# Kernel optimization log

Hardware: AMD Instinct MI355X
Metric: run time of the kernel (lower is better)

The kernel has to match this reference:

```python
import jax, jax.numpy as jnp
import numpy as np

B, L, D, H, N, F_, DM = 16, 2048, 128, 4, 4, 129, 16
DK = D // H
DFF = 2 * D
INT = int(np.sqrt(D))  # 11
V = F_ + 1


def _uinit(key, shape, fan):
    s = float(np.sqrt(6.0 / fan))
    return jax.random.uniform(key, shape, jnp.float32, -s, s)


def setup_inputs() -> dict:
    key = jax.random.key(0)
    ks = jax.random.split(key, 24)
    return {
        "values": jax.random.normal(ks[0], (B, L), jnp.float32),
        "times": jax.random.uniform(ks[1], (B, L), jnp.float32),
        "variables": jax.random.randint(ks[2], (B, L), 0, F_),
        "input_mask": jax.random.randint(ks[3], (B, L), 0, 2).astype(bool),
        "demographics": jax.random.normal(ks[4], (B, DM), jnp.float32),
        # CVE time
        "W1t": _uinit(ks[5], (1, INT), 1 + INT), "b1t": jnp.zeros((INT,), jnp.float32),
        "W2t": _uinit(ks[6], (INT, D), INT + D),
        # CVE value
        "W1v": _uinit(ks[7], (1, INT), 1 + INT), "b1v": jnp.zeros((INT,), jnp.float32),
        "W2v": _uinit(ks[8], (INT, D), INT + D),
        # variable embedding table
        "var_table": jax.random.normal(ks[9], (V, D), jnp.float32),
        # transformer stacks (init_proj: uniform(-s, s), s = sqrt(6/(fan_in+fan_out)) of last two dims)
        "Wq": _uinit(ks[10], (N, H, D, DK), D + DK),
        "Wk": _uinit(ks[11], (N, H, D, DK), D + DK),
        "Wv": _uinit(ks[12], (N, H, D, DK), D + DK),
        "Wo": _uinit(ks[13], (N, D, D), 2 * D),
        "W1": _uinit(ks[14], (N, D, DFF), D + DFF), "b1": jnp.zeros((N, 1, 1, DFF), jnp.float32),
        "W2": _uinit(ks[15], (N, DFF, D), DFF + D), "b2": jnp.zeros((N, 1, 1, D), jnp.float32),
        # fusion attention
        "Wf": _uinit(ks[16], (D, D), 2 * D), "bf": jnp.zeros((D,), jnp.float32),
        "uf": _uinit(ks[17], (D, 1), D + 1),
        # demographics MLP
        "Wd1": _uinit(ks[18], (DM, 2 * D), DM + 2 * D), "bd1": jnp.zeros((2 * D,), jnp.float32),
        "Wd2": _uinit(ks[19], (2 * D, D), 3 * D), "bd2": jnp.zeros((D,), jnp.float32),
        # head: forecast_fc
        "Wh": _uinit(ks[20], (2 * D, F_), 2 * D + F_), "bh": jnp.zeros((F_,), jnp.float32),
    }


def reference(values, times, variables, input_mask, demographics,
              W1t, b1t, W2t, W1v, b1v, W2v, var_table,
              Wq, Wk, Wv, Wo, W1, b1, W2, b2,
              Wf, bf, uf, Wd1, bd1, Wd2, bd2, Wh, bh):
    FMIN = jnp.finfo(values.dtype).min
    # demographics MLP
    demo = jnp.tanh(demographics @ Wd1 + bd1) @ Wd2 + bd2
    # continuous value embeddings (CVE): x -> tanh(x*W1 + b1) @ W2
    te = jnp.tanh(times[..., None] * W1t[0] + b1t) @ W2t    # [B,L,D]
    ve = jnp.tanh(values[..., None] * W1v[0] + b1v) @ W2v   # [B,L,D]
    x = te + ve + var_table[variables]                      # [B,L,D]
    # additive pairwise mask (finite FMIN, matches torch finfo.min semantics)
    m = input_mask
    pair = m[:, :, None] & m[:, None, :]                    # [B,L,L]
    addm = jnp.where(pair[:, None, :, :], 0.0, FMIN)        # [B,1,L,L]
    n_layers = Wq.shape[0]
    bsz, max_len, _ = x.shape
    for i in range(n_layers):
        q = jnp.einsum('bld,hde->bhle', x, Wq[i])
        k = jnp.einsum('bld,hde->bhle', x, Wk[i])
        v = jnp.einsum('bld,hde->bhle', x, Wv[i])
        A = jnp.einsum('bhle,bhke->bhlk', q, k) + addm      # NOTE: no 1/sqrt(dk) scaling, as in source
        A = jax.nn.softmax(A, axis=-1)
        o = jnp.einsum('bhlk,bhke->blhe', A, v).reshape(bsz, max_len, -1)
        x = o @ Wo[i] + x
        f = jax.nn.gelu(x @ W1[i] + b1[i], approximate=False)
        x = f @ W2[i] + b2[i] + x
    # fusion attention pooling
    att = (jnp.tanh(x @ Wf + bf) @ uf)[:, :, 0]             # [B,L]
    att = att + jnp.where(m, 0.0, FMIN)
    w = jax.nn.softmax(att, axis=-1)
    ts = jnp.sum(x * w[:, :, None], axis=1)                 # [B,D]
    emb = jnp.concatenate([ts, demo], axis=-1)              # [B,2D]
    return emb @ Wh + bh                                    # [B,features_num]
```

## Files before the change

### kernel.cpp

```cpp
#include <hip/hip_runtime.h>
#include <hip/hip_bf16.h>
#include <math.h>

#define B_   16
#define L_   2048
#define D_   128
#define H_   4
#define NL_  4
#define DK_  32
#define DFF_ 256
#define INTD_ 11
#define F_OUT 129
#define DM_  16
#define FMINV (-3.402823466e38f)
#define LOG2E 1.4426950408889634f

#define BL_  (B_*L_)
#define SZ_X (BL_*D_)

#define PSTR 68

#define WT_Q 0
#define WT_K 16384
#define WT_V 32768
#define WT_O 49152
#define WT_1 65536
#define WT_2 98304
#define WT_TOT 131072

typedef __attribute__((ext_vector_type(8))) short bf16x8;
typedef __attribute__((ext_vector_type(4))) float f32x4;

#if __has_builtin(__builtin_amdgcn_exp2f)
#define EXP2F(x) __builtin_amdgcn_exp2f(x)
#else
#define EXP2F(x) __expf(0.69314718055994531f*(x))
#endif

static __device__ __forceinline__ short f2bf(float x) {
    union { __hip_bfloat16 h; short s; } u;
    u.h = __float2bfloat16(x);
    return u.s;
}
static __device__ __forceinline__ float bf2f(short s) {
    union { __hip_bfloat16 h; short t; } u;
    u.t = s;
    return __bfloat162float(u.h);
}
static __device__ __forceinline__ void split2(float v, short& h, short& l) {
    h = f2bf(v); l = f2bf(v - bf2f(h));
}
static __device__ __forceinline__ void split_trunc(float v, short& h, short& l) {
    unsigned u = __float_as_uint(v);
    h = (short)(u >> 16);
    float r = v - __uint_as_float(u & 0xffff0000u);
    l = (short)(__float_as_uint(r) >> 16);
}

__global__ __launch_bounds__(256)
void compact_kernel(const int* __restrict__ mask, int* __restrict__ pos,
                    int* __restrict__ kcount, float* __restrict__ cfm,
                    float* __restrict__ x)
{
    int b = blockIdx.x, t = threadIdx.x;
    int lane = t & 63, w = t >> 6;
    __shared__ int wsum[4];
    __shared__ int tot_s;
    int mv[8], loc[8], s = 0;
#pragma unroll
    for (int i = 0; i < 8; ++i) {
        mv[i] = mask[b*L_ + t*8 + i];
        loc[i] = s;
        s += mv[i];
    }
    int v = s;
#pragma unroll
    for (int d = 1; d < 64; d <<= 1) {
        int y = __shfl_up(v, d);
        if (lane >= d) v += y;
    }
    int excl = v - s;
    if (lane == 63) wsum[w] = v;
    __syncthreads();
    int wbase = 0;
    for (int i = 0; i < w; ++i) wbase += wsum[i];
    int base = wbase + excl;
#pragma unroll
    for (int i = 0; i < 8; ++i)
        pos[b*L_ + t*8 + i] = mv[i] ? (base + loc[i]) : -1;
    if (t == 255) { kcount[b] = base + s; tot_s = base + s; }
    __syncthreads();
    int tot = tot_s;
    for (int l = t; l < L_; l += 256) cfm[b*L_ + l] = (l < tot) ? 0.0f : FMINV;
    int end = (tot + 63) & ~63;
    int nz = (end - tot) * D_;
    for (int i = t; i < nz; i += 256)
        x[((size_t)(b*2048 + tot))*D_ + i] = 0.0f;
}

__global__ __launch_bounds__(128)
void embed_kernel(const float* __restrict__ values, const float* __restrict__ times,
                  const int* __restrict__ variables, const int* __restrict__ pos,
                  const float* __restrict__ W1t, const float* __restrict__ b1t,
                  const float* __restrict__ W2t,
                  const float* __restrict__ W1v, const float* __restrict__ b1v,
                  const float* __restrict__ W2v,
                  const float* __restrict__ var_table, float* __restrict__ x)
{
    int bl = blockIdx.x;
    int p  = pos[bl];
    if (p < 0) return;
    int t  = threadIdx.x;
    __shared__ float th[INTD_], vh[INTD_];
    if (t < INTD_)                th[t]    = tanhf(times[bl]  * W1t[t]    + b1t[t]);
    if (t >= 64 && t < 64+INTD_)  vh[t-64] = tanhf(values[bl] * W1v[t-64] + b1v[t-64]);
    __syncthreads();
    int var = variables[bl];
    float acc = var_table[var*D_ + t];
#pragma unroll
    for (int i = 0; i < INTD_; ++i)
        acc += th[i]*W2t[i*D_ + t] + vh[i]*W2v[i*D_ + t];
    x[((size_t)((bl >> 11)*2048 + p))*D_ + t] = acc;
}

__global__ __launch_bounds__(256)
void split_all_kernel(const float* __restrict__ Wq, const float* __restrict__ Wk,
                      const float* __restrict__ Wv, const float* __restrict__ Wo,
                      const float* __restrict__ W1, const float* __restrict__ W2,
                      const float* __restrict__ Wf,
                      short* __restrict__ hi, short* __restrict__ lo)
{
    int gidx = blockIdx.x*256 + threadIdx.x;
    float v;
    if (gidx < NL_*131072) {
        int layer = gidx >> 17;
        int idx   = gidx & 131071;
        if (idx < 49152) {
            int which = idx >> 14;
            int r = idx & 16383;
            int col = r >> 7, k = r & 127;
            int h = col >> 5, e = col & 31;
            const float* src = ((which == 0) ? Wq : (which == 1) ? Wk : Wv)
                               + (size_t)layer*H_*D_*DK_;
            v = src[(h*D_ + k)*DK_ + e];
        } else if (idx < 65536) {
            int r = idx - 49152;
            int col = r >> 7, k = r & 127;
            v = Wo[(size_t)layer*D_*D_ + k*D_ + col];
        } else if (idx < 98304) {
            int r = idx - 65536;
            int col = r >> 7, k = r & 127;
            v = W1[(size_t)layer*D_*DFF_ + k*DFF_ + col];
        } else {
            int r = idx - 98304;
            int col = r >> 8, k = r & 255;
            v = W2[(size_t)layer*DFF_*D_ + k*D_ + col];
        }
    } else {
        int r = gidx - NL_*131072;
        int col = r >> 7, k = r & 127;
        v = Wf[k*D_ + col];
    }
    short h2, l2; split2(v, h2, l2);
    hi[gidx] = h2; lo[gidx] = l2;
}

__global__ __launch_bounds__(256)
void gemm_qkv_fused(const float* __restrict__ A, const short* __restrict__ Whi,
                    const short* __restrict__ Wlo, const int* __restrict__ kcount,
                    float* __restrict__ qout,
                    short* __restrict__ khi, short* __restrict__ klo,
                    short* __restrict__ vhiT, short* __restrict__ vloT)
{
    const int row0 = blockIdx.x * 64;
    const int bb = row0 >> 11;
    if ((row0 & 2047) >= ((kcount[bb] + 63) & ~63)) return;
    const int sec = blockIdx.y;

    __shared__ short Ahi[64*136];
    __shared__ short Alo[64*136];
    const int t = threadIdx.x;
    const int w = t >> 6, lane = t & 63;
    const int m = lane & 15, qd = lane >> 4;

#pragma unroll
    for (int i = 0; i < 8; ++i) {
        int r = (t >> 5) + 8*i;
        int c = (t & 31) * 4;
        float4 av = *(const float4*)(A + (size_t)(row0 + r)*D_ + c);
        short4 hi4, lo4;
        split2(av.x, hi4.x, lo4.x);
        split2(av.y, hi4.y, lo4.y);
        split2(av.z, hi4.z, lo4.z);
        split2(av.w, hi4.w, lo4.w);
        *(short4*)&Ahi[r*136 + c] = hi4;
        *(short4*)&Alo[r*136 + c] = lo4;
    }
    __syncthreads();

    const short* Wh = Whi + sec*16384;
    const short* Wl = Wlo + sec*16384;
    f32x4 acc[4][2];
#pragma unroll
    for (int r4 = 0; r4 < 4; ++r4)
#pragma unroll
        for (int j = 0; j < 2; ++j) acc[r4][j] = (f32x4){0,0,0,0};

#pragma unroll
    for (int ks = 0; ks < 4; ++ks) {
        bf16x8 wh[2], wl[2];
#pragma unroll
        for (int j = 0; j < 2; ++j) {
            size_t wi = (size_t)(32*w + 16*j + m)*D_ + 32*ks + 8*qd;
            wh[j] = *(const bf16x8*)(Wh + wi);
            wl[j] = *(const bf16x8*)(Wl + wi);
        }
#pragma unroll
        for (int r4 = 0; r4 < 4; ++r4) {
            bf16x8 ah = *(const bf16x8*)&Ahi[(16*r4 + m)*136 + 32*ks + 8*qd];
            bf16x8 al = *(const bf16x8*)&Alo[(16*r4 + m)*136 + 32*ks + 8*qd];
#pragma unroll
            for (int j = 0; j < 2; ++j) {
                acc[r4][j] = __builtin_amdgcn_mfma_f32_16x16x32_bf16(wh[j], ah, acc[r4][j], 0, 0, 0);
                acc[r4][j] = __builtin_amdgcn_mfma_f32_16x16x32_bf16(wh[j], al, acc[r4][j], 0, 0, 0);
                acc[r4][j] = __builtin_amdgcn_mfma_f32_16x16x32_bf16(wl[j], ah, acc[r4][j], 0, 0, 0);
            }
        }
    }

#pragma unroll
    for (int r4 = 0; r4 < 4; ++r4) {
        int row = row0 + 16*r4 + m;
        int l = row & 2047;
#pragma unroll
        for (int j = 0; j < 2; ++j) {
            int col = 32*w + 16*j + 4*qd;
            f32x4 v = acc[r4][j];
            if (sec == 0) {
                float4 sv = {v[0], v[1], v[2], v[3]};
                *(float4*)(qout + (size_t)row*D_ + col) = sv;
            } else if (sec == 1) {
                size_t idx = ((size_t)((bb*4 + w)*2048 + l))*32 + (col & 31);
                short4 hi4, lo4;
                split2(v[0], hi4.x, lo4.x);
                split2(v[1], hi4.y, lo4.y);
                split2(v[2], hi4.z, lo4.z);
                split2(v[3], hi4.w, lo4.w);
                *(short4*)(khi + idx) = hi4;
                *(short4*)(klo + idx) = lo4;
            } else {
                size_t basep = (size_t)(bb*4 + w)*32;
#pragma unroll
                for (int e = 0; e < 4; ++e) {
                    int d = 16*j + 4*qd + e;
                    short hh, ll; split2(v[e], hh, ll);
                    vhiT[(basep + d)*2048 + l] = hh;
                    vloT[(basep + d)*2048 + l] = ll;
                }
            }
        }
    }
}

__global__ __launch_bounds__(256)
void attn_mfma_kernel(const float* __restrict__ q,
                      const short* __restrict__ khi, const short* __restrict__ klo,
                      const short* __restrict__ vhiT, const short* __restrict__ vloT,
                      const int* __restrict__ kcount, const float* __restrict__ cfm,
                      float* __restrict__ opart, float* __restrict__ mlm,
                      float* __restrict__ mll)
{
    __shared__ short KhiS[64*32];
    __shared__ short KloS[64*32];
    __shared__ short Vthi[32*72];
    __shared__ short Vtlo[32*72];
    __shared__ short Ps[4][16*PSTR];
    __shared__ float kmf[64];
    __shared__ float al_ls[4][16];

    const int t    = threadIdx.x;
    const int w    = t >> 6;
    const int lane = t & 63;
    const int m    = lane & 15;
    const int qd   = lane >> 4;
    const int qt = blockIdx.x, b = blockIdx.z;
    const int h = blockIdx.y & 3, half = blockIdx.y >> 2;

    const int Kb = kcount[b];
    if (qt*64 >= Kb) return;
    const int nt = (Kb + 63) >> 6;
    const int ntH = (nt + 1) >> 1;
    const int kt0 = half * ntH;
    const int kt1 = (kt0 + ntH < nt) ? (kt0 + ntH) : nt;
    const size_t mlbase = (((size_t)(b*4 + h))*2 + half)*2048;

    if (kt0 >= kt1) {
        if (lane < 16) {
            mlm[mlbase + qt*64 + 16*w + lane] = FMINV;
            mll[mlbase + qt*64 + 16*w + lane] = 0.0f;
        }
        return;
    }

    const size_t hd = ((size_t)(b*4 + h))*2048*32;
    const int vd = t >> 3;
    const int vk = (t & 7) * 8;
    const size_t vbase = ((size_t)(b*4 + h)*32 + vd)*2048 + vk;

    const int qrow = qt*64 + 16*w + m;
    const float* qp = q + ((size_t)(b*L_ + qrow))*D_ + h*DK_ + 8*qd;
    float qf[8];
    *(float4*)&qf[0] = *(const float4*)qp;
    *(float4*)&qf[4] = *(const float4*)(qp + 4);
    bf16x8 qhi, qlo;
#pragma unroll
    for (int j = 0; j < 8; ++j) {
        float qs = qf[j] * LOG2E;
        short hs = f2bf(qs);
        qhi[j] = hs;
        qlo[j] = f2bf(qs - bf2f(hs));
    }

    bf16x8 pkh, pkl, pvh, pvl;
    float4 pmask = {0,0,0,0};
    {
        const size_t gk = hd + (size_t)kt0*64*32 + t*8;
        pkh = *(const bf16x8*)(khi + gk);
        pkl = *(const bf16x8*)(klo + gk);
        pvh = *(const bf16x8*)(vhiT + vbase + (size_t)kt0*64);
        pvl = *(const bf16x8*)(vloT + vbase + (size_t)kt0*64);
        if (t < 16) pmask = ((const float4*)(cfm + (size_t)b*L_ + (size_t)kt0*64))[t];
    }

    float m_old = -INFINITY, l_run = 0.0f;
    f32x4 o_acc[2] = {{0,0,0,0},{0,0,0,0}};

    for (int kt = kt0; kt < kt1; ++kt) {
        __syncthreads();
        *(bf16x8*)&KhiS[t*8] = pkh;
        *(bf16x8*)&KloS[t*8] = pkl;
        *(bf16x8*)&Vthi[vd*72 + vk] = pvh;
        *(bf16x8*)&Vtlo[vd*72 + vk] = pvl;
        if (t < 16) ((float4*)kmf)[t] = pmask;
        __syncthreads();
        if (kt + 1 < kt1) {
            const size_t gk = hd + (size_t)(kt+1)*64*32 + t*8;
            pkh = *(const bf16x8*)(khi + gk);
            pkl = *(const bf16x8*)(klo + gk);
            pvh = *(const bf16x8*)(vhiT + vbase + (size_t)(kt+1)*64);
            pvl = *(const bf16x8*)(vloT + vbase + (size_t)(kt+1)*64);
            if (t < 16) pmask = ((const float4*)(cfm + (size_t)b*L_ + (size_t)(kt+1)*64))[t];
        }

        f32x4 sf[4];
#pragma unroll
        for (int k4 = 0; k4 < 4; ++k4) {
            bf16x8 ka = *(const bf16x8*)&KhiS[(16*k4 + m)*32 + 8*qd];
            bf16x8 kl = *(const bf16x8*)&KloS[(16*k4 + m)*32 + 8*qd];
            f32x4 c = {0,0,0,0};
            c = __builtin_amdgcn_mfma_f32_16x16x32_bf16(ka, qhi, c, 0, 0, 0);
            c = __builtin_amdgcn_mfma_f32_16x16x32_bf16(ka, qlo, c, 0, 0, 0);
            c = __builtin_amdgcn_mfma_f32_16x16x32_bf16(kl, qhi, c, 0, 0, 0);
            sf[k4] = c;
        }

        float sv[16];
#pragma unroll
        for (int k4 = 0; k4 < 4; ++k4) {
            float4 kmv = *(const float4*)&kmf[16*k4 + 4*qd];
            sv[4*k4+0] = sf[k4][0] + kmv.x;
            sv[4*k4+1] = sf[k4][1] + kmv.y;
            sv[4*k4+2] = sf[k4][2] + kmv.z;
            sv[4*k4+3] = sf[k4][3] + kmv.w;
        }

        float tmax = sv[0];
#pragma unroll
        for (int j = 1; j < 16; ++j) tmax = fmaxf(tmax, sv[j]);
        tmax = fmaxf(tmax, __shfl_xor(tmax, 16));
        tmax = fmaxf(tmax, __shfl_xor(tmax, 32));
        float mnew  = fmaxf(m_old, tmax);
        float alpha = EXP2F(m_old - mnew);
        float psum = 0.0f;
        short pbh[16], pbl[16];
#pragma unroll
        for (int j = 0; j < 16; ++j) {
            float p = EXP2F(sv[j] - mnew);
            psum += p;
            split_trunc(p, pbh[j], pbl[j]);
        }
        psum += __shfl_xor(psum, 16);
        psum += __shfl_xor(psum, 32);
        l_run = l_run * alpha + psum;
        m_old = mnew;

#pragma unroll
        for (int k4 = 0; k4 < 4; ++k4) {
            short4 s4h;
            s4h.x = pbh[4*k4+0]; s4h.y = pbh[4*k4+1]; s4h.z = pbh[4*k4+2]; s4h.w = pbh[4*k4+3];
            *(short4*)&Ps[w][m*PSTR + 16*k4 + 4*qd] = s4h;
        }
        if (lane < 16) al_ls[w][lane] = alpha;

        {
            float4 alr = *(const float4*)&al_ls[w][4*qd];
            o_acc[0][0]*=alr.x; o_acc[0][1]*=alr.y; o_acc[0][2]*=alr.z; o_acc[0][3]*=alr.w;
            o_acc[1][0]*=alr.x; o_acc[1][1]*=alr.y; o_acc[1][2]*=alr.z; o_acc[1][3]*=alr.w;
        }
#pragma unroll
        for (int s = 0; s < 2; ++s) {
            bf16x8 pah = *(const bf16x8*)&Ps[w][m*PSTR + 32*s + 8*qd];
#pragma unroll
            for (int tp = 0; tp < 2; ++tp) {
                bf16x8 vh = *(const bf16x8*)&Vthi[(16*tp + m)*72 + 32*s + 8*qd];
                bf16x8 vl = *(const bf16x8*)&Vtlo[(16*tp + m)*72 + 32*s + 8*qd];
                o_acc[tp] = __builtin_amdgcn_mfma_f32_16x16x32_bf16(pah, vh, o_acc[tp], 0, 0, 0);
                o_acc[tp] = __builtin_amdgcn_mfma_f32_16x16x32_bf16(pah, vl, o_acc[tp], 0, 0, 0);
            }
        }
#pragma unroll
        for (int k4 = 0; k4 < 4; ++k4) {
            short4 s4l;
            s4l.x = pbl[4*k4+0]; s4l.y = pbl[4*k4+1]; s4l.z = pbl[4*k4+2]; s4l.w = pbl[4*k4+3];
            *(short4*)&Ps[w][m*PSTR + 16*k4 + 4*qd] = s4l;
        }
#pragma unroll
        for (int s = 0; s < 2; ++s) {
            bf16x8 pal = *(const bf16x8*)&Ps[w][m*PSTR + 32*s + 8*qd];
#pragma unroll
            for (int tp = 0; tp < 2; ++tp) {
                bf16x8 vh = *(const bf16x8*)&Vthi[(16*tp + m)*72 + 32*s + 8*qd];
                o_acc[tp] = __builtin_amdgcn_mfma_f32_16x16x32_bf16(pal, vh, o_acc[tp], 0, 0, 0);
            }
        }
    }

    if (lane < 16) {
        mlm[mlbase + qt*64 + 16*w + lane] = m_old;
        mll[mlbase + qt*64 + 16*w + lane] = l_run;
    }
    float* ob = opart + (size_t)half*SZ_X;
#pragma unroll
    for (int tp = 0; tp < 2; ++tp)
#pragma unroll
        for (int r = 0; r < 4; ++r)
            ob[((size_t)(b*L_ + qt*64 + 16*w + 4*qd + r))*D_ + h*DK_ + 16*tp + m] =
                o_acc[tp][r];
}

__global__ __launch_bounds__(256)
void wo_ffn1_kernel(const float* __restrict__ opart, const float* __restrict__ mlm,
                    const float* __restrict__ mll,
                    const short* __restrict__ WhiO, const short* __restrict__ WloO,
                    const short* __restrict__ Whi1, const short* __restrict__ Wlo1,
                    const float* __restrict__ b1,
                    const int* __restrict__ kcount, float* __restrict__ x,
                    float* __restrict__ hb)
{
    const int row0 = blockIdx.x * 64;
    const int bb = row0 >> 11;
    if ((row0 & 2047) >= ((kcount[bb] + 63) & ~63)) return;

    __shared__ short Ahi[64*136];
    __shared__ short Alo[64*136];
    const int t = threadIdx.x;
    const int w = t >> 6, lane = t & 63;
    const int m = lane & 15, qd = lane >> 4;

#pragma unroll
    for (int i = 0; i < 8; ++i) {
        int r = (t >> 5) + 8*i;
        int c = (t & 31) * 4;
        int row = row0 + r;
        int l = row & 2047;
        int h = c >> 5;
        size_t i0 = (((size_t)(bb*4 + h))*2 + 0)*2048 + l;
        size_t i1 = i0 + 2048;
        float m0 = mlm[i0], m1 = mlm[i1];
        float l0 = mll[i0], l1 = mll[i1];
        float M  = fmaxf(m0, m1);
        float w0 = EXP2F(m0 - M), w1 = EXP2F(m1 - M);
        float inv = 1.0f / (l0*w0 + l1*w1);
        float s0 = w0 * inv, s1 = w1 * inv;
        float4 o0 = *(const float4*)(opart + (size_t)row*D_ + c);
        float4 o1 = *(const float4*)(opart + (size_t)(BL_ + row)*D_ + c);
        float4 av;
        av.x = s0*o0.x + s1*o1.x;
        av.y = s0*o0.y + s1*o1.y;
        av.z = s0*o0.z + s1*o1.z;
        av.w = s0*o0.w + s1*o1.w;
        short4 hi4, lo4;
        split2(av.x, hi4.x, lo4.x);
        split2(av.y, hi4.y, lo4.y);
        split2(av.z, hi4.z, lo4.z);
        split2(av.w, hi4.w, lo4.w);
        *(short4*)&Ahi[r*136 + c] = hi4;
        *(short4*)&Alo[r*136 + c] = lo4;
    }
    __syncthreads();

    f32x4 acc[4][2];
#pragma unroll
    for (int r4 = 0; r4 < 4; ++r4)
#pragma unroll
        for (int j = 0; j < 2; ++j) acc[r4][j] = (f32x4){0,0,0,0};
#pragma unroll
    for (int ks = 0; ks < 4; ++ks) {
        bf16x8 wh[2], wl[2];
#pragma unroll
        for (int j = 0; j < 2; ++j) {
            size_t wi = (size_t)(32*w + 16*j + m)*D_ + 32*ks + 8*qd;
            wh[j] = *(const bf16x8*)(WhiO + wi);
            wl[j] = *(const bf16x8*)(WloO + wi);
        }
#pragma unroll
        for (int r4 = 0; r4 < 4; ++r4) {
            bf16x8 ah = *(const bf16x8*)&Ahi[(16*r4 + m)*136 + 32*ks + 8*qd];
            bf16x8 al = *(const bf16x8*)&Alo[(16*r4 + m)*136 + 32*ks + 8*qd];
#pragma unroll
            for (int j = 0; j < 2; ++j) {
                acc[r4][j] = __builtin_amdgcn_mfma_f32_16x16x32_bf16(wh[j], ah, acc[r4][j], 0, 0, 0);
                acc[r4][j] = __builtin_amdgcn_mfma_f32_16x16x32_bf16(wh[j], al, acc[r4][j], 0, 0, 0);
                acc[r4][j] = __builtin_amdgcn_mfma_f32_16x16x32_bf16(wl[j], ah, acc[r4][j], 0, 0, 0);
            }
        }
    }

#pragma unroll
    for (int r4 = 0; r4 < 4; ++r4) {
        int row = row0 + 16*r4 + m;
#pragma unroll
        for (int j = 0; j < 2; ++j) {
            int col = 32*w + 16*j + 4*qd;
            float4 rv = *(const float4*)(x + (size_t)row*D_ + col);
            acc[r4][j][0] += rv.x; acc[r4][j][1] += rv.y;
            acc[r4][j][2] += rv.z; acc[r4][j][3] += rv.w;
            float4 sv = {acc[r4][j][0], acc[r4][j][1], acc[r4][j][2], acc[r4][j][3]};
            *(float4*)(x + (size_t)row*D_ + col) = sv;
        }
    }
    __syncthreads();

#pragma unroll
    for (int r4 = 0; r4 < 4; ++r4) {
#pragma unroll
        for (int j = 0; j < 2; ++j) {
            int col = 32*w + 16*j + 4*qd;
            short4 hi4, lo4;
            split2(acc[r4][j][0], hi4.x, lo4.x);
            split2(acc[r4][j][1], hi4.y, lo4.y);
            split2(acc[r4][j][2], hi4.z, lo4.z);
            split2(acc[r4][j][3], hi4.w, lo4.w);
            *(short4*)&Ahi[(16*r4 + m)*136 + col] = hi4;
            *(short4*)&Alo[(16*r4 + m)*136 + col] = lo4;
        }
    }
    __syncthreads();

    f32x4 a2[4][4];
#pragma unroll
    for (int r4 = 0; r4 < 4; ++r4)
#pragma unroll
        for (int jj = 0; jj < 4; ++jj) a2[r4][jj] = (f32x4){0,0,0,0};
#pragma unroll
    for (int ks = 0; ks < 4; ++ks) {
        bf16x8 wh[4], wl[4];
#pragma unroll
        for (int jj = 0; jj < 4; ++jj) {
            size_t wi = (size_t)(64*w + 16*jj + m)*D_ + 32*ks + 8*qd;
            wh[jj] = *(const bf16x8*)(Whi1 + wi);
            wl[jj] = *(const bf16x8*)(Wlo1 + wi);
        }
#pragma unroll
        for (int r4 = 0; r4 < 4; ++r4) {
            bf16x8 ah = *(const bf16x8*)&Ahi[(16*r4 + m)*136 + 32*ks + 8*qd];
            bf16x8 al = *(const bf16x8*)&Alo[(16*r4 + m)*136 + 32*ks + 8*qd];
#pragma unroll
            for (int jj = 0; jj < 4; ++jj) {
                a2[r4][jj] = __builtin_amdgcn_mfma_f32_16x16x32_bf16(wh[jj], ah, a2[r4][jj], 0, 0, 0);
                a2[r4][jj] = __builtin_amdgcn_mfma_f32_16x16x32_bf16(wh[jj], al, a2[r4][jj], 0, 0, 0);
                a2[r4][jj] = __builtin_amdgcn_mfma_f32_16x16x32_bf16(wl[jj], ah, a2[r4][jj], 0, 0, 0);
            }
        }
    }

#pragma unroll
    for (int r4 = 0; r4 < 4; ++r4) {
        int row = row0 + 16*r4 + m;
#pragma unroll
        for (int jj = 0; jj < 4; ++jj) {
            int col = 64*w + 16*jj + 4*qd;
            f32x4 v = a2[r4][jj];
            float4 bv = *(const float4*)(b1 + col);
            v[0] += bv.x; v[1] += bv.y; v[2] += bv.z; v[3] += bv.w;
#pragma unroll
            for (int e = 0; e < 4; ++e)
                v[e] = 0.5f * v[e] * (1.0f + erff(v[e] * 0.70710678118654752f));
            float4 sv = {v[0], v[1], v[2], v[3]};
            *(float4*)(hb + (size_t)row*DFF_ + col) = sv;
        }
    }
}

template<int TAIL>
__global__ __launch_bounds__(256)
void ffn2_next_kernel(const float* __restrict__ hb,
                      const short* __restrict__ Whi2, const short* __restrict__ Wlo2,
                      const float* __restrict__ b2,
                      const short* __restrict__ WhiN, const short* __restrict__ WloN,
                      const float* __restrict__ bfv, const float* __restrict__ uf,
                      const float* __restrict__ cfm,
                      const int* __restrict__ kcount, float* __restrict__ x,
                      float* __restrict__ qout,
                      short* __restrict__ khi, short* __restrict__ klo,
                      short* __restrict__ vhiT, short* __restrict__ vloT,
                      float* __restrict__ attb)
{
    const int row0 = blockIdx.x * 64;
    const int bb = row0 >> 11;
    if ((row0 & 2047) >= ((kcount[bb] + 63) & ~63)) return;

    __shared__ short Ahi[64*136];
    __shared__ short Alo[64*136];
    __shared__ float part[64][16];
    const int t = threadIdx.x;
    const int w = t >> 6, lane = t & 63;
    const int m = lane & 15, qd = lane >> 4;

    f32x4 acc[4][2];
#pragma unroll
    for (int r4 = 0; r4 < 4; ++r4)
#pragma unroll
        for (int j = 0; j < 2; ++j) acc[r4][j] = (f32x4){0,0,0,0};

    for (int kb = 0; kb < DFF_; kb += 128) {
        if (kb) __syncthreads();
#pragma unroll
        for (int i = 0; i < 8; ++i) {
            int r = (t >> 5) + 8*i;
            int c = (t & 31) * 4;
            float4 av = *(const float4*)(hb + (size_t)(row0 + r)*DFF_ + kb + c);
            short4 hi4, lo4;
            split2(av.x, hi4.x, lo4.x);
            split2(av.y, hi4.y, lo4.y);
            split2(av.z, hi4.z, lo4.z);
            split2(av.w, hi4.w, lo4.w);
            *(short4*)&Ahi[r*136 + c] = hi4;
            *(short4*)&Alo[r*136 + c] = lo4;
        }
        __syncthreads();

#pragma unroll
        for (int ks = 0; ks < 4; ++ks) {
            bf16x8 wh[2], wl[2];
#pragma unroll
            for (int j = 0; j < 2; ++j) {
                size_t wi = (size_t)(32*w + 16*j + m)*DFF_ + kb + 32*ks + 8*qd;
                wh[j] = *(const bf16x8*)(Whi2 + wi);
                wl[j] = *(const bf16x8*)(Wlo2 + wi);
            }
#pragma unroll
            for (int r4 = 0; r4 < 4; ++r4) {
                bf16x8 ah = *(const bf16x8*)&Ahi[(16*r4 + m)*136 + 32*ks + 8*qd];
                bf16x8 al = *(const bf16x8*)&Alo[(16*r4 + m)*136 + 32*ks + 8*qd];
#pragma unroll
                for (int j = 0; j < 2; ++j) {
                    acc[r4][j] = __builtin_amdgcn_mfma_f32_16x16x32_bf16(wh[j], ah, acc[r4][j], 0, 0, 0);
                    acc[r4][j] = __builtin_amdgcn_mfma_f32_16x16x32_bf16(wh[j], al, acc[r4][j], 0, 0, 0);
                    acc[r4][j] = __builtin_amdgcn_mfma_f32_16x16x32_bf16(wl[j], ah, acc[r4][j], 0, 0, 0);
                }
            }
        }
    }

#pragma unroll
    for (int r4 = 0; r4 < 4; ++r4) {
        int row = row0 + 16*r4 + m;
#pragma unroll
        for (int j = 0; j < 2; ++j) {
            int col = 32*w + 16*j + 4*qd;
            float4 bv = *(const float4*)(b2 + col);
            float4 rv = *(const float4*)(x + (size_t)row*D_ + col);
            acc[r4][j][0] += bv.x + rv.x; acc[r4][j][1] += bv.y + rv.y;
            acc[r4][j][2] += bv.z + rv.z; acc[r4][j][3] += bv.w + rv.w;
            float4 sv = {acc[r4][j][0], acc[r4][j][1], acc[r4][j][2], acc[r4][j][3]};
            *(float4*)(x + (size_t)row*D_ + col) = sv;
        }
    }
    __syncthreads();

#pragma unroll
    for (int r4 = 0; r4 < 4; ++r4) {
#pragma unroll
        for (int j = 0; j < 2; ++j) {
            int col = 32*w + 16*j + 4*qd;
            short4 hi4, lo4;
            split2(acc[r4][j][0], hi4.x, lo4.x);
            split2(acc[r4][j][1], hi4.y, lo4.y);
            split2(acc[r4][j][2], hi4.z, lo4.z);
            split2(acc[r4][j][3], hi4.w, lo4.w);
            *(short4*)&Ahi[(16*r4 + m)*136 + col] = hi4;
            *(short4*)&Alo[(16*r4 + m)*136 + col] = lo4;
        }
    }
    __syncthreads();

    if (TAIL == 0) {
#pragma unroll
        for (int sec = 0; sec < 3; ++sec) {
            const short* Wh = WhiN + sec*16384;
            const short* Wl = WloN + sec*16384;
            f32x4 a3[4][2];
#pragma unroll
            for (int r4 = 0; r4 < 4; ++r4)
#pragma unroll
                for (int j = 0; j < 2; ++j) a3[r4][j] = (f32x4){0,0,0,0};
#pragma unroll
            for (int ks = 0; ks < 4; ++ks) {
                bf16x8 wh[2], wl[2];
#pragma unroll
                for (int j = 0; j < 2; ++j) {
                    size_t wi = (size_t)(32*w + 16*j + m)*D_ + 32*ks + 8*qd;
                    wh[j] = *(const bf16x8*)(Wh + wi);
                    wl[j] = *(const bf16x8*)(Wl + wi);
                }
#pragma unroll
                for (int r4 = 0; r4 < 4; ++r4) {
                    bf16x8 ah = *(const bf16x8*)&Ahi[(16*r4 + m)*136 + 32*ks + 8*qd];
                    bf16x8 al = *(const bf16x8*)&Alo[(16*r4 + m)*136 + 32*ks + 8*qd];
#pragma unroll
                    for (int j = 0; j < 2; ++j) {
                        a3[r4][j] = __builtin_amdgcn_mfma_f32_16x16x32_bf16(wh[j], ah, a3[r4][j], 0, 0, 0);
                        a3[r4][j] = __builtin_amdgcn_mfma_f32_16x16x32_bf16(wh[j], al, a3[r4][j], 0, 0, 0);
                        a3[r4][j] = __builtin_amdgcn_mfma_f32_16x16x32_bf16(wl[j], ah, a3[r4][j], 0, 0, 0);
                    }
                }
            }
#pragma unroll
            for (int r4 = 0; r4 < 4; ++r4) {
                int row = row0 + 16*r4 + m;
                int l = row & 2047;
#pragma unroll
                for (int j = 0; j < 2; ++j) {
                    int col = 32*w + 16*j + 4*qd;
                    f32x4 v = a3[r4][j];
                    if (sec == 0) {
                        float4 sv = {v[0], v[1], v[2], v[3]};
                        *(float4*)(qout + (size_t)row*D_ + col) = sv;
                    } else if (sec == 1) {
                        size_t idx = ((size_t)((bb*4 + w)*2048 + l))*32 + (col & 31);
                        short4 hi4, lo4;
                        split2(v[0], hi4.x, lo4.x);
                        split2(v[1], hi4.y, lo4.y);
                        split2(v[2], hi4.z, lo4.z);
                        split2(v[3], hi4.w, lo4.w);
                        *(short4*)(khi + idx) = hi4;
                        *(short4*)(klo + idx) = lo4;
                    } else {
                        size_t basep = (size_t)(bb*4 + w)*32;
#pragma unroll
                        for (int e = 0; e < 4; ++e) {
                            int d = 16*j + 4*qd + e;
                            short hh, ll; split2(v[e], hh, ll);
                            vhiT[(basep + d)*2048 + l] = hh;
                            vloT[(basep + d)*2048 + l] = ll;
                        }
                    }
                }
            }
        }
    } else {
        f32x4 a3[4][2];
#pragma unroll
        for (int r4 = 0; r4 < 4; ++r4)
#pragma unroll
            for (int j = 0; j < 2; ++j) a3[r4][j] = (f32x4){0,0,0,0};
#pragma unroll
        for (int ks = 0; ks < 4; ++ks) {
            bf16x8 wh[2], wl[2];
#pragma unroll
            for (int j = 0; j < 2; ++j) {
                size_t wi = (size_t)(32*w + 16*j + m)*D_ + 32*ks + 8*qd;
                wh[j] = *(const bf16x8*)(WhiN + wi);
                wl[j] = *(const bf16x8*)(WloN + wi);
            }
#pragma unroll
            for (int r4 = 0; r4 < 4; ++r4) {
                bf16x8 ah = *(const bf16x8*)&Ahi[(16*r4 + m)*136 + 32*ks + 8*qd];
                bf16x8 al = *(const bf16x8*)&Alo[(16*r4 + m)*136 + 32*ks + 8*qd];
#pragma unroll
                for (int j = 0; j < 2; ++j) {
                    a3[r4][j] = __builtin_amdgcn_mfma_f32_16x16x32_bf16(wh[j], ah, a3[r4][j], 0, 0, 0);
                    a3[r4][j] = __builtin_amdgcn_mfma_f32_16x16x32_bf16(wh[j], al, a3[r4][j], 0, 0, 0);
                    a3[r4][j] = __builtin_amdgcn_mfma_f32_16x16x32_bf16(wl[j], ah, a3[r4][j], 0, 0, 0);
                }
            }
        }
#pragma unroll
        for (int r4 = 0; r4 < 4; ++r4) {
            float dotp = 0.0f;
#pragma unroll
            for (int j = 0; j < 2; ++j) {
                int col = 32*w + 16*j + 4*qd;
                f32x4 v = a3[r4][j];
                float4 bv = *(const float4*)(bfv + col);
                v[0] += bv.x; v[1] += bv.y; v[2] += bv.z; v[3] += bv.w;
#pragma unroll
                for (int e = 0; e < 4; ++e) v[e] = tanhf(v[e]);
                float4 uv = *(const float4*)(uf + col);
                dotp += v[0]*uv.x + v[1]*uv.y + v[2]*uv.z + v[3]*uv.w;
            }
            part[16*r4 + m][4*w + qd] = dotp;
        }
        __syncthreads();
        if (t < 64) {
            float s = 0.0f;
#pragma unroll
            for (int i = 0; i < 16; ++i) s += part[t][i];
            attb[row0 + t] = s + cfm[row0 + t];
        }
    }
}

__global__ __launch_bounds__(256)
void pool_stats_kernel(const float* __restrict__ att, const int* __restrict__ kcount,
                       float* __restrict__ p)
{
    int b = blockIdx.x, t = threadIdx.x;
    int lim = (kcount[b] + 63) & ~63;
    __shared__ float red[4];
    __shared__ float a_s[L_];

    float m = -INFINITY;
    for (int l = t; l < L_; l += 256) {
        float a = (l < lim) ? att[b*L_ + l] : FMINV;
        a_s[l] = a;
        m = fmaxf(m, a);
    }
#pragma unroll
    for (int s = 1; s < 64; s <<= 1) m = fmaxf(m, __shfl_xor(m, s));
    if ((t & 63) == 0) red[t >> 6] = m;
    __syncthreads();
    m = fmaxf(fmaxf(red[0], red[1]), fmaxf(red[2], red[3]));
    __syncthreads();

    float s = 0.0f;
    for (int l = t; l < L_; l += 256) s += __expf(a_s[l] - m);
#pragma unroll
    for (int st = 1; st < 64; st <<= 1) s += __shfl_xor(s, st);
    if ((t & 63) == 0) red[t >> 6] = s;
    __syncthreads();
    s = red[0] + red[1] + red[2] + red[3];
    float inv = 1.0f / s;
    for (int l = t; l < L_; l += 256)
        p[b*L_ + l] = (l < lim) ? __expf(a_s[l] - m) * inv : 0.0f;
}

__global__ __launch_bounds__(128)
void pool_partial_kernel(const float* __restrict__ p, const float* __restrict__ x,
                         float* __restrict__ part)
{
    int c = blockIdx.x, b = blockIdx.y, d = threadIdx.x;
    const float* xb = x + ((size_t)(b*L_ + c*128))*D_ + d;
    const float* pb = p + b*L_ + c*128;
    float acc = 0.0f;
#pragma unroll 4
    for (int i = 0; i < 128; ++i) acc += pb[i] * xb[(size_t)i*D_];
    part[((size_t)b*16 + c)*D_ + d] = acc;
}

__global__ __launch_bounds__(256)
void head_kernel(const float* __restrict__ part, const float* __restrict__ demog,
                 const float* __restrict__ Wd1, const float* __restrict__ bd1,
                 const float* __restrict__ Wd2, const float* __restrict__ bd2,
                 const float* __restrict__ Wh, const float* __restrict__ bh,
                 float* __restrict__ out)
{
    int b = blockIdx.x, t = threadIdx.x;
    __shared__ float tss[128];
    __shared__ float hs1[256];
    __shared__ float dems[128];
    if (t < 128) {
        float s = 0.0f;
#pragma unroll
        for (int c = 0; c < 16; ++c) s += part[((size_t)b*16 + c)*D_ + t];
        tss[t] = s;
    }
    {
        float a = bd1[t];
#pragma unroll
        for (int kk = 0; kk < DM_; ++kk) a += demog[b*DM_ + kk] * Wd1[kk*(2*D_) + t];
        hs1[t] = tanhf(a);
    }
    __syncthreads();
    if (t < 128) {
        float a = bd2[t];
        for (int kk = 0; kk < 2*D_; ++kk) a += hs1[kk] * Wd2[kk*D_ + t];
        dems[t] = a;
    }
    __syncthreads();
    if (t >= F_OUT) return;
    float acc = bh[t];
    for (int k2 = 0; k2 < D_; ++k2) acc += tss[k2]  * Wh[k2*F_OUT + t];
    for (int k2 = 0; k2 < D_; ++k2) acc += dems[k2] * Wh[(D_+k2)*F_OUT + t];
    out[b*F_OUT + t] = acc;
}

extern "C" void kernel_launch(void* const* d_in, const int* in_sizes, int n_in,
                              void* d_out, int out_size, void* d_ws, size_t ws_size,
                              hipStream_t stream)
{
    (void)in_sizes; (void)n_in; (void)out_size; (void)ws_size;
    const float* values       = (const float*)d_in[0];
    const float* times        = (const float*)d_in[1];
    const int*   variables    = (const int*)  d_in[2];
    const int*   input_mask   = (const int*)  d_in[3];
    const float* demographics = (const float*)d_in[4];
    const float* W1t = (const float*)d_in[5];
    const float* b1t = (const float*)d_in[6];
    const float* W2t = (const float*)d_in[7];
    const float* W1v = (const float*)d_in[8];
    const float* b1v = (const float*)d_in[9];
    const float* W2v = (const float*)d_in[10];
    const float* var_table = (const float*)d_in[11];
    const float* Wq  = (const float*)d_in[12];
    const float* Wk  = (const float*)d_in[13];
    const float* Wv  = (const float*)d_in[14];
    const float* Wo  = (const float*)d_in[15];
    const float* W1  = (const float*)d_in[16];
    const float* b1  = (const float*)d_in[17];
    const float* W2  = (const float*)d_in[18];
    const float* b2  = (const float*)d_in[19];
    const float* Wf  = (const float*)d_in[20];
    const float* bfv = (const float*)d_in[21];
    const float* uf  = (const float*)d_in[22];
    const float* Wd1 = (const float*)d_in[23];
    const float* bd1 = (const float*)d_in[24];
    const float* Wd2 = (const float*)d_in[25];
    const float* bd2 = (const float*)d_in[26];
    const float* Wh  = (const float*)d_in[27];
    const float* bhv = (const float*)d_in[28];
    float* out = (float*)d_out;

    float* ws     = (float*)d_ws;
    float* x      = ws;
    float* qb     = ws + (size_t)SZ_X;
    float* region = ws + (size_t)2*SZ_X;
    short* khi    = (short*)region;
    short* klo    = khi + (size_t)SZ_X;
    short* vhiT   = klo + (size_t)SZ_X;
    short* vloT   = vhiT + (size_t)SZ_X;
    float* attb   = ws + (size_t)4*SZ_X;
    float* attp   = attb + BL_;
    float* partb  = attp + BL_;
    short* wt_hi  = (short*)(partb + B_*16*D_);
    short* wt_lo  = wt_hi + ((size_t)NL_*WT_TOT + 16384);
    int*   posb   = (int*)(wt_lo + ((size_t)NL_*WT_TOT + 16384));
    int*   kcountb= posb + BL_;
    float* cfmb   = (float*)(kcountb + B_ + 3);
    float* opart  = cfmb + BL_;
    float* mlm    = opart + (size_t)2*SZ_X;
    float* mll    = mlm + (size_t)B_*H_*2*2048;
    float* hb     = mll + (size_t)B_*H_*2*2048;
    short* wfhi   = wt_hi + (size_t)NL_*WT_TOT;
    short* wflo   = wt_lo + (size_t)NL_*WT_TOT;

    compact_kernel<<<B_, 256, 0, stream>>>(input_mask, posb, kcountb, cfmb, x);
    embed_kernel<<<BL_, 128, 0, stream>>>(values, times, variables, posb,
                                          W1t, b1t, W2t, W1v, b1v, W2v,
                                          var_table, x);
    split_all_kernel<<<(NL_*131072 + 16384)/256, 256, 0, stream>>>(
        Wq, Wk, Wv, Wo, W1, W2, Wf, wt_hi, wt_lo);

    gemm_qkv_fused<<<dim3(BL_/64, 3), 256, 0, stream>>>(x,
        wt_hi + 0*WT_TOT, wt_lo + 0*WT_TOT, kcountb, qb, khi, klo, vhiT, vloT);

    for (int i = 0; i < NL_; ++i) {
        short* whL = wt_hi + (size_t)i*WT_TOT;
        short* wlL = wt_lo + (size_t)i*WT_TOT;
        attn_mfma_kernel<<<dim3(L_/64, H_*2, B_), 256, 0, stream>>>(qb, khi, klo,
            vhiT, vloT, kcountb, cfmb, opart, mlm, mll);
        wo_ffn1_kernel<<<BL_/64, 256, 0, stream>>>(opart, mlm, mll,
            whL+WT_O, wlL+WT_O, whL+WT_1, wlL+WT_1, b1 + i*DFF_,
            kcountb, x, hb);
        if (i < NL_ - 1) {
            short* whN = wt_hi + (size_t)(i+1)*WT_TOT;
            short* wlN = wt_lo + (size_t)(i+1)*WT_TOT;
            ffn2_next_kernel<0><<<BL_/64, 256, 0, stream>>>(hb,
                whL+WT_2, wlL+WT_2, b2 + i*D_, whN, wlN,
                nullptr, nullptr, nullptr, kcountb, x,
                qb, khi, klo, vhiT, vloT, nullptr);
        } else {
            ffn2_next_kernel<1><<<BL_/64, 256, 0, stream>>>(hb,
                whL+WT_2, wlL+WT_2, b2 + i*D_, wfhi, wflo,
                bfv, uf, cfmb, kcountb, x,
                nullptr, nullptr, nullptr, nullptr, nullptr, attb);
        }
    }

    pool_stats_kernel<<<B_, 256, 0, stream>>>(attb, kcountb, attp);
    pool_partial_kernel<<<dim3(16, B_), 128, 0, stream>>>(attp, x, partb);
    head_kernel<<<B_, 256, 0, stream>>>(partb, demographics, Wd1, bd1, Wd2, bd2,
                                        Wh, bhv, out);
}
```

Baseline: 794.8 us.

## Pad K smem, drop mask/alpha LDS, set MFMA priority, halve GEMM row tiles

The attention kernel pads the K shared-memory stride to 36 to cut bank conflicts. It loads the key mask directly from global memory instead of staging it in LDS, and broadcasts alpha with shuffles instead of an LDS round trip. It also wraps the MFMA sections in s_setprio and turns the max and sum reductions into trees. Separately, the Wo/FFN1 and FFN2/next-QKV kernels now process 32-row tiles instead of 64, doubling the grid for more parallelism at the cost of re-reading weights per block. The early-exit check still rounds kcount up to 64, so tiles past the valid length may do extra work.

```diff
diff --git a/kernel.cpp b/kernel.cpp
--- a/kernel.cpp
+++ b/kernel.cpp
@@ -19,6 +19,7 @@
 #define SZ_X (BL_*D_)
 
 #define PSTR 68
+#define KSTR 36
 
 #define WT_Q 0
 #define WT_K 16384
@@ -270,13 +271,11 @@
                       float* __restrict__ opart, float* __restrict__ mlm,
                       float* __restrict__ mll)
 {
-    __shared__ short KhiS[64*32];
-    __shared__ short KloS[64*32];
+    __shared__ short KhiS[64*KSTR];
+    __shared__ short KloS[64*KSTR];
     __shared__ short Vthi[32*72];
     __shared__ short Vtlo[32*72];
     __shared__ short Ps[4][16*PSTR];
-    __shared__ float kmf[64];
-    __shared__ float al_ls[4][16];
 
     const int t    = threadIdx.x;
     const int w    = t >> 6;
@@ -306,6 +305,7 @@
     const int vd = t >> 3;
     const int vk = (t & 7) * 8;
     const size_t vbase = ((size_t)(b*4 + h)*32 + vd)*2048 + vk;
+    const int kw_off = (t >> 2)*KSTR + (t & 3)*8;
 
     const int qrow = qt*64 + 16*w + m;
     const float* qp = q + ((size_t)(b*L_ + qrow))*D_ + h*DK_ + 8*qd;
@@ -322,14 +322,12 @@
     }
 
     bf16x8 pkh, pkl, pvh, pvl;
-    float4 pmask = {0,0,0,0};
     {
         const size_t gk = hd + (size_t)kt0*64*32 + t*8;
         pkh = *(const bf16x8*)(khi + gk);
         pkl = *(const bf16x8*)(klo + gk);
         pvh = *(const bf16x8*)(vhiT + vbase + (size_t)kt0*64);
         pvl = *(const bf16x8*)(vloT + vbase + (size_t)kt0*64);
-        if (t < 16) pmask = ((const float4*)(cfm + (size_t)b*L_ + (size_t)kt0*64))[t];
     }
 
     float m_old = -INFINITY, l_run = 0.0f;
@@ -337,11 +335,10 @@
 
     for (int kt = kt0; kt < kt1; ++kt) {
         __syncthreads();
-        *(bf16x8*)&KhiS[t*8] = pkh;
-        *(bf16x8*)&KloS[t*8] = pkl;
+        *(bf16x8*)&KhiS[kw_off] = pkh;
+        *(bf16x8*)&KloS[kw_off] = pkl;
         *(bf16x8*)&Vthi[vd*72 + vk] = pvh;
         *(bf16x8*)&Vtlo[vd*72 + vk] = pvl;
-        if (t < 16) ((float4*)kmf)[t] = pmask;
         __syncthreads();
         if (kt + 1 < kt1) {
             const size_t gk = hd + (size_t)(kt+1)*64*32 + t*8;
@@ -349,46 +346,61 @@
             pkl = *(const bf16x8*)(klo + gk);
             pvh = *(const bf16x8*)(vhiT + vbase + (size_t)(kt+1)*64);
             pvl = *(const bf16x8*)(vloT + vbase + (size_t)(kt+1)*64);
-            if (t < 16) pmask = ((const float4*)(cfm + (size_t)b*L_ + (size_t)(kt+1)*64))[t];
-        }
+        }
+
+        const float* cfmp = cfm + (size_t)b*L_ + (size_t)kt*64 + 4*qd;
+        float4 kmv4[4];
+#pragma unroll
+        for (int k4 = 0; k4 < 4; ++k4)
+            kmv4[k4] = *(const float4*)(cfmp + 16*k4);
 
         f32x4 sf[4];
+        __builtin_amdgcn_s_setprio(1);
 #pragma unroll
         for (int k4 = 0; k4 < 4; ++k4) {
-            bf16x8 ka = *(const bf16x8*)&KhiS[(16*k4 + m)*32 + 8*qd];
-            bf16x8 kl = *(const bf16x8*)&KloS[(16*k4 + m)*32 + 8*qd];
+            bf16x8 ka = *(const bf16x8*)&KhiS[(16*k4 + m)*KSTR + 8*qd];
+            bf16x8 kl = *(const bf16x8*)&KloS[(16*k4 + m)*KSTR + 8*qd];
             f32x4 c = {0,0,0,0};
             c = __builtin_amdgcn_mfma_f32_16x16x32_bf16(ka, qhi, c, 0, 0, 0);
             c = __builtin_amdgcn_mfma_f32_16x16x32_bf16(ka, qlo, c, 0, 0, 0);
             c = __builtin_amdgcn_mfma_f32_16x16x32_bf16(kl, qhi, c, 0, 0, 0);
             sf[k4] = c;
         }
+        __builtin_amdgcn_s_setprio(0);
 
         float sv[16];
 #pragma unroll
         for (int k4 = 0; k4 < 4; ++k4) {
-            float4 kmv = *(const float4*)&kmf[16*k4 + 4*qd];
-            sv[4*k4+0] = sf[k4][0] + kmv.x;
-            sv[4*k4+1] = sf[k4][1] + kmv.y;
-            sv[4*k4+2] = sf[k4][2] + kmv.z;
-            sv[4*k4+3] = sf[k4][3] + kmv.w;
-        }
-
-        float tmax = sv[0];
-#pragma unroll
-        for (int j = 1; j < 16; ++j) tmax = fmaxf(tmax, sv[j]);
+            sv[4*k4+0] = sf[k4][0] + kmv4[k4].x;
+            sv[4*k4+1] = sf[k4][1] + kmv4[k4].y;
+            sv[4*k4+2] = sf[k4][2] + kmv4[k4].z;
+            sv[4*k4+3] = sf[k4][3] + kmv4[k4].w;
+        }
+
+        float mx8[8];
+#pragma unroll
+        for (int j = 0; j < 8; ++j) mx8[j] = fmaxf(sv[2*j], sv[2*j+1]);
+#pragma unroll
+        for (int j = 0; j < 4; ++j) mx8[j] = fmaxf(mx8[j], mx8[j+4]);
+        float tmax = fmaxf(fmaxf(mx8[0], mx8[1]), fmaxf(mx8[2], mx8[3]));
         tmax = fmaxf(tmax, __shfl_xor(tmax, 16));
         tmax = fmaxf(tmax, __shfl_xor(tmax, 32));
         float mnew  = fmaxf(m_old, tmax);
         float alpha = EXP2F(m_old - mnew);
-        float psum = 0.0f;
+        float pj[16];
         short pbh[16], pbl[16];
 #pragma unroll
         for (int j = 0; j < 16; ++j) {
             float p = EXP2F(sv[j] - mnew);
-            psum += p;
+            pj[j] = p;
             split_trunc(p, pbh[j], pbl[j]);
         }
+        float ps8[8];
+#pragma unroll
+        for (int j = 0; j < 8; ++j) ps8[j] = pj[2*j] + pj[2*j+1];
+#pragma unroll
+        for (int j = 0; j < 4; ++j) ps8[j] = ps8[j] + ps8[j+4];
+        float psum = (ps8[0] + ps8[1]) + (ps8[2] + ps8[3]);
         psum += __shfl_xor(psum, 16);
         psum += __shfl_xor(psum, 32);
         l_run = l_run * alpha + psum;
@@ -400,13 +412,16 @@
             s4h.x = pbh[4*k4+0]; s4h.y = pbh[4*k4+1]; s4h.z = pbh[4*k4+2]; s4h.w = pbh[4*k4+3];
             *(short4*)&Ps[w][m*PSTR + 16*k4 + 4*qd] = s4h;
         }
-        if (lane < 16) al_ls[w][lane] = alpha;
 
         {
-            float4 alr = *(const float4*)&al_ls[w][4*qd];
-            o_acc[0][0]*=alr.x; o_acc[0][1]*=alr.y; o_acc[0][2]*=alr.z; o_acc[0][3]*=alr.w;
-            o_acc[1][0]*=alr.x; o_acc[1][1]*=alr.y; o_acc[1][2]*=alr.z; o_acc[1][3]*=alr.w;
-        }
+            float a0 = __shfl(alpha, 4*qd + 0);
+            float a1 = __shfl(alpha, 4*qd + 1);
+            float a2 = __shfl(alpha, 4*qd + 2);
+            float a3 = __shfl(alpha, 4*qd + 3);
+            o_acc[0][0]*=a0; o_acc[0][1]*=a1; o_acc[0][2]*=a2; o_acc[0][3]*=a3;
+            o_acc[1][0]*=a0; o_acc[1][1]*=a1; o_acc[1][2]*=a2; o_acc[1][3]*=a3;
+        }
+        __builtin_amdgcn_s_setprio(1);
 #pragma unroll
         for (int s = 0; s < 2; ++s) {
             bf16x8 pah = *(const bf16x8*)&Ps[w][m*PSTR + 32*s + 8*qd];
@@ -433,6 +448,7 @@
                 o_acc[tp] = __builtin_amdgcn_mfma_f32_16x16x32_bf16(pal, vh, o_acc[tp], 0, 0, 0);
             }
         }
+        __builtin_amdgcn_s_setprio(0);
     }
 
     if (lane < 16) {
@@ -457,18 +473,18 @@
                     const int* __restrict__ kcount, float* __restrict__ x,
                     float* __restrict__ hb)
 {
-    const int row0 = blockIdx.x * 64;
+    const int row0 = blockIdx.x * 32;
     const int bb = row0 >> 11;
     if ((row0 & 2047) >= ((kcount[bb] + 63) & ~63)) return;
 
-    __shared__ short Ahi[64*136];
-    __shared__ short Alo[64*136];
+    __shared__ short Ahi[32*136];
+    __shared__ short Alo[32*136];
     const int t = threadIdx.x;
     const int w = t >> 6, lane = t & 63;
     const int m = lane & 15, qd = lane >> 4;
 
 #pragma unroll
-    for (int i = 0; i < 8; ++i) {
+    for (int i = 0; i < 4; ++i) {
         int r = (t >> 5) + 8*i;
         int c = (t & 31) * 4;
         int row = row0 + r;
@@ -499,9 +515,9 @@
     }
     __syncthreads();
 
-    f32x4 acc[4][2];
-#pragma unroll
-    for (int r4 = 0; r4 < 4; ++r4)
+    f32x4 acc[2][2];
+#pragma unroll
+    for (int r4 = 0; r4 < 2; ++r4)
 #pragma unroll
         for (int j = 0; j < 2; ++j) acc[r4][j] = (f32x4){0,0,0,0};
 #pragma unroll
@@ -514,7 +530,7 @@
             wl[j] = *(const bf16x8*)(WloO + wi);
         }
 #pragma unroll
-        for (int r4 = 0; r4 < 4; ++r4) {
+        for (int r4 = 0; r4 < 2; ++r4) {
             bf16x8 ah = *(const bf16x8*)&Ahi[(16*r4 + m)*136 + 32*ks + 8*qd];
             bf16x8 al = *(const bf16x8*)&Alo[(16*r4 + m)*136 + 32*ks + 8*qd];
 #pragma unroll
@@ -527,7 +543,7 @@
     }
 
 #pragma unroll
-    for (int r4 = 0; r4 < 4; ++r4) {
+    for (int r4 = 0; r4 < 2; ++r4) {
         int row = row0 + 16*r4 + m;
 #pragma unroll
         for (int j = 0; j < 2; ++j) {
@@ -542,7 +558,7 @@
     __syncthreads();
 
 #pragma unroll
-    for (int r4 = 0; r4 < 4; ++r4) {
+    for (int r4 = 0; r4 < 2; ++r4) {
 #pragma unroll
         for (int j = 0; j < 2; ++j) {
             int col = 32*w + 16*j + 4*qd;
@@ -557,9 +573,9 @@
     }
     __syncthreads();
 
-    f32x4 a2[4][4];
-#pragma unroll
-    for (int r4 = 0; r4 < 4; ++r4)
+    f32x4 a2[2][4];
+#pragma unroll
+    for (int r4 = 0; r4 < 2; ++r4)
 #pragma unroll
         for (int jj = 0; jj < 4; ++jj) a2[r4][jj] = (f32x4){0,0,0,0};
 #pragma unroll
@@ -572,7 +588,7 @@
             wl[jj] = *(const bf16x8*)(Wlo1 + wi);
         }
 #pragma unroll
-        for (int r4 = 0; r4 < 4; ++r4) {
+        for (int r4 = 0; r4 < 2; ++r4) {
             bf16x8 ah = *(const bf16x8*)&Ahi[(16*r4 + m)*136 + 32*ks + 8*qd];
             bf16x8 al = *(const bf16x8*)&Alo[(16*r4 + m)*136 + 32*ks + 8*qd];
 #pragma unroll
@@ -585,7 +601,7 @@
     }
 
 #pragma unroll
-    for (int r4 = 0; r4 < 4; ++r4) {
+    for (int r4 = 0; r4 < 2; ++r4) {
         int row = row0 + 16*r4 + m;
 #pragma unroll
         for (int jj = 0; jj < 4; ++jj) {
@@ -616,27 +632,27 @@
                       short* __restrict__ vhiT, short* __restrict__ vloT,
                       float* __restrict__ attb)
 {
-    const int row0 = blockIdx.x * 64;
+    const int row0 = blockIdx.x * 32;
     const int bb = row0 >> 11;
     if ((row0 & 2047) >= ((kcount[bb] + 63) & ~63)) return;
 
-    __shared__ short Ahi[64*136];
-    __shared__ short Alo[64*136];
-    __shared__ float part[64][16];
+    __shared__ short Ahi[32*136];
+    __shared__ short Alo[32*136];
+    __shared__ float part[32][16];
     const int t = threadIdx.x;
     const int w = t >> 6, lane = t & 63;
     const int m = lane & 15, qd = lane >> 4;
 
-    f32x4 acc[4][2];
-#pragma unroll
-    for (int r4 = 0; r4 < 4; ++r4)
+    f32x4 acc[2][2];
+#pragma unroll
+    for (int r4 = 0; r4 < 2; ++r4)
 #pragma unroll
         for (int j = 0; j < 2; ++j) acc[r4][j] = (f32x4){0,0,0,0};
 
     for (int kb = 0; kb < DFF_; kb += 128) {
         if (kb) __syncthreads();
 #pragma unroll
-        for (int i = 0; i < 8; ++i) {
+        for (int i = 0; i < 4; ++i) {
             int r = (t >> 5) + 8*i;
             int c = (t & 31) * 4;
             float4 av = *(const float4*)(hb + (size_t)(row0 + r)*DFF_ + kb + c);
@@ -660,7 +676,7 @@
                 wl[j] = *(const bf16x8*)(Wlo2 + wi);
             }
 #pragma unroll
-            for (int r4 = 0; r4 < 4; ++r4) {
+            for (int r4 = 0; r4 < 2; ++r4) {
                 bf16x8 ah = *(const bf16x8*)&Ahi[(16*r4 + m)*136 + 32*ks + 8*qd];
                 bf16x8 al = *(const bf16x8*)&Alo[(16*r4 + m)*136 + 32*ks + 8*qd];
 #pragma unroll
@@ -674,7 +690,7 @@
     }
 
 #pragma unroll
-    for (int r4 = 0; r4 < 4; ++r4) {
+    for (int r4 = 0; r4 < 2; ++r4) {
         int row = row0 + 16*r4 + m;
 #pragma unroll
         for (int j = 0; j < 2; ++j) {
@@ -690,7 +706,7 @@
     __syncthreads();
 
 #pragma unroll
-    for (int r4 = 0; r4 < 4; ++r4) {
+    for (int r4 = 0; r4 < 2; ++r4) {
 #pragma unroll
         for (int j = 0; j < 2; ++j) {
             int col = 32*w + 16*j + 4*qd;
@@ -710,9 +726,9 @@
         for (int sec = 0; sec < 3; ++sec) {
             const short* Wh = WhiN + sec*16384;
             const short* Wl = WloN + sec*16384;
-            f32x4 a3[4][2];
-#pragma unroll
-            for (int r4 = 0; r4 < 4; ++r4)
+            f32x4 a3[2][2];
+#pragma unroll
+            for (int r4 = 0; r4 < 2; ++r4)
 #pragma unroll
                 for (int j = 0; j < 2; ++j) a3[r4][j] = (f32x4){0,0,0,0};
 #pragma unroll
@@ -725,7 +741,7 @@
                     wl[j] = *(const bf16x8*)(Wl + wi);
                 }
 #pragma unroll
-                for (int r4 = 0; r4 < 4; ++r4) {
+                for (int r4 = 0; r4 < 2; ++r4) {
                     bf16x8 ah = *(const bf16x8*)&Ahi[(16*r4 + m)*136 + 32*ks + 8*qd];
                     bf16x8 al = *(const bf16x8*)&Alo[(16*r4 + m)*136 + 32*ks + 8*qd];
 #pragma unroll
@@ -737,7 +753,7 @@
                 }
             }
 #pragma unroll
-            for (int r4 = 0; r4 < 4; ++r4) {
+            for (int r4 = 0; r4 < 2; ++r4) {
                 int row = row0 + 16*r4 + m;
                 int l = row & 2047;
 #pragma unroll
@@ -770,9 +786,9 @@
             }
         }
     } else {
-        f32x4 a3[4][2];
-#pragma unroll
-        for (int r4 = 0; r4 < 4; ++r4)
+        f32x4 a3[2][2];
+#pragma unroll
+        for (int r4 = 0; r4 < 2; ++r4)
 #pragma unroll
             for (int j = 0; j < 2; ++j) a3[r4][j] = (f32x4){0,0,0,0};
 #pragma unroll
@@ -785,7 +801,7 @@
                 wl[j] = *(const bf16x8*)(WloN + wi);
             }
 #pragma unroll
-            for (int r4 = 0; r4 < 4; ++r4) {
+            for (int r4 = 0; r4 < 2; ++r4) {
                 bf16x8 ah = *(const bf16x8*)&Ahi[(16*r4 + m)*136 + 32*ks + 8*qd];
                 bf16x8 al = *(const bf16x8*)&Alo[(16*r4 + m)*136 + 32*ks + 8*qd];
 #pragma unroll
@@ -797,7 +813,7 @@
             }
         }
 #pragma unroll
-        for (int r4 = 0; r4 < 4; ++r4) {
+        for (int r4 = 0; r4 < 2; ++r4) {
             float dotp = 0.0f;
 #pragma unroll
             for (int j = 0; j < 2; ++j) {
@@ -813,7 +829,7 @@
             part[16*r4 + m][4*w + qd] = dotp;
         }
         __syncthreads();
-        if (t < 64) {
+        if (t < 32) {
             float s = 0.0f;
 #pragma unroll
             for (int i = 0; i < 16; ++i) s += part[t][i];
@@ -980,18 +996,18 @@
         short* wlL = wt_lo + (size_t)i*WT_TOT;
         attn_mfma_kernel<<<dim3(L_/64, H_*2, B_), 256, 0, stream>>>(qb, khi, klo,
             vhiT, vloT, kcountb, cfmb, opart, mlm, mll);
-        wo_ffn1_kernel<<<BL_/64, 256, 0, stream>>>(opart, mlm, mll,
+        wo_ffn1_kernel<<<BL_/32, 256, 0, stream>>>(opart, mlm, mll,
             whL+WT_O, wlL+WT_O, whL+WT_1, wlL+WT_1, b1 + i*DFF_,
             kcountb, x, hb);
         if (i < NL_ - 1) {
             short* whN = wt_hi + (size_t)(i+1)*WT_TOT;
             short* wlN = wt_lo + (size_t)(i+1)*WT_TOT;
-            ffn2_next_kernel<0><<<BL_/64, 256, 0, stream>>>(hb,
+            ffn2_next_kernel<0><<<BL_/32, 256, 0, stream>>>(hb,
                 whL+WT_2, wlL+WT_2, b2 + i*D_, whN, wlN,
                 nullptr, nullptr, nullptr, kcountb, x,
                 qb, khi, klo, vhiT, vloT, nullptr);
         } else {
-            ffn2_next_kernel<1><<<BL_/64, 256, 0, stream>>>(hb,
+            ffn2_next_kernel<1><<<BL_/32, 256, 0, stream>>>(hb,
                 whL+WT_2, wlL+WT_2, b2 + i*D_, wfhi, wflo,
                 bfv, uf, cfmb, kcountb, x,
                 nullptr, nullptr, nullptr, nullptr, nullptr, attb);
```

Measured after the change: 866.0 us. 1.09x slower.
